# Performance work log

Hardware: AMD Instinct MI355X
Metric: run time of the kernel (lower is better)

## Reference

```python
import jax, jax.numpy as jnp
import numpy as np

TEMPERATURE = 1.0 / 0.07  # fixed (temperature_trainable=False)
B, D = 256, 65536


def setup_inputs() -> dict:
    key = jax.random.key(0)
    kA, kB = jax.random.split(key)
    feat_A = jax.random.normal(kA, (B, D), dtype=jnp.float32)
    feat_B = jax.random.normal(kB, (B, D), dtype=jnp.float32)
    # L2-normalize (standard for contrastive features; keeps exp(logits) finite)
    feat_A = feat_A / jnp.linalg.norm(feat_A, axis=-1, keepdims=True)
    feat_B = feat_B / jnp.linalg.norm(feat_B, axis=-1, keepdims=True)
    return {"feat_A": feat_A, "feat_B": feat_B}


def reference(feat_A, feat_B):
    # logits[i, j] = <A_i, B_j> * temperature   -- [B, B]
    logits = jnp.einsum("id,jd->ij", feat_A, feat_B) * TEMPERATURE
    pos_logits = jnp.diagonal(logits)  # [B]
    # margin=0.0, dcl=False, index=None -> neg_mask is all True, so
    # log(sum_j exp(logits)) is a full-row/col logsumexp (stable form of exp->sum->log)
    neg_A2B = jax.nn.logsumexp(logits, axis=1)  # A -> B classification
    neg_B2A = jax.nn.logsumexp(logits, axis=0)  # B -> A classification
    loss_A2B = jnp.mean(neg_A2B - pos_logits)
    loss_B2A = jnp.mean(neg_B2A - pos_logits)
    return (loss_A2B + loss_B2A) * 0.5
```

## Files before the change

### kernel.cpp

```cpp
#include <hip/hip_runtime.h>
#include <hip/hip_bf16.h>


#define D_DIM 65536
#define B_DIM 256
#define LDK 72

constexpr float TEMP = 1.0f / 0.07f;

typedef short short8 __attribute__((ext_vector_type(8)));
typedef float floatx4 __attribute__((ext_vector_type(4)));

__device__ inline unsigned short f2bf(float f) {
  unsigned u = __builtin_bit_cast(unsigned, f);
  unsigned rounding = 0x7fffu + ((u >> 16) & 1u);
  return (unsigned short)((u + rounding) >> 16);
}

__device__ inline void st_bf16x4(unsigned short* dst, float4 v) {
  uint2 u;
  u.x = (unsigned)f2bf(v.x) | ((unsigned)f2bf(v.y) << 16);
  u.y = (unsigned)f2bf(v.z) | ((unsigned)f2bf(v.w) << 16);
  *(uint2*)dst = u;
}

__global__ __launch_bounds__(256, 2) void gemm_splitk(
    const float* __restrict__ A, const float* __restrict__ Bm,
    float* __restrict__ partials, int Kc) {
  const int bid = blockIdx.x;
  const int mt = (bid & 1) * 128;
  const int nt = ((bid >> 1) & 1) * 128;
  const int chunk = bid >> 2;
  const size_t k0 = (size_t)chunk * (size_t)Kc;

  __shared__ unsigned short As[128][LDK];
  __shared__ unsigned short Bs[128][LDK];

  const int t = threadIdx.x;
  const int lane = t & 63;
  const int w = t >> 6;
  const int wm = (w & 1) * 64;
  const int wn = (w >> 1) * 64;

  const int lr = t >> 4;
  const int lc = (t & 15) * 4;

  const float* Abase = A + (size_t)(mt + lr) * D_DIM + k0 + lc;
  const float* Bbase = Bm + (size_t)(nt + lr) * D_DIM + k0 + lc;

  floatx4 acc[4][4];
#pragma unroll
  for (int mb = 0; mb < 4; ++mb)
#pragma unroll
    for (int nb = 0; nb < 4; ++nb) acc[mb][nb] = (floatx4)0.f;

  float4 ra[8], rb[8];
  const int nst = Kc >> 6;

#pragma unroll
  for (int p = 0; p < 8; ++p) {
    ra[p] = *(const float4*)(Abase + (size_t)p * 16 * D_DIM);
    rb[p] = *(const float4*)(Bbase + (size_t)p * 16 * D_DIM);
  }

  for (int s = 0; s < nst; ++s) {
#pragma unroll
    for (int p = 0; p < 8; ++p) {
      st_bf16x4(&As[lr + p * 16][lc], ra[p]);
      st_bf16x4(&Bs[lr + p * 16][lc], rb[p]);
    }
    __syncthreads();

    if (s + 1 < nst) {
      const float* Ap = Abase + (size_t)(s + 1) * 64;
      const float* Bp = Bbase + (size_t)(s + 1) * 64;
#pragma unroll
      for (int p = 0; p < 8; ++p) {
        ra[p] = *(const float4*)(Ap + (size_t)p * 16 * D_DIM);
        rb[p] = *(const float4*)(Bp + (size_t)p * 16 * D_DIM);
      }
    }

#pragma unroll
    for (int ks = 0; ks < 64; ks += 32) {
      short8 af[4], bf[4];
      const int ko = ks + (lane >> 4) * 8;
#pragma unroll
      for (int mb = 0; mb < 4; ++mb)
        af[mb] = *(const short8*)&As[wm + mb * 16 + (lane & 15)][ko];
#pragma unroll
      for (int nb = 0; nb < 4; ++nb)
        bf[nb] = *(const short8*)&Bs[wn + nb * 16 + (lane & 15)][ko];
#pragma unroll
      for (int mb = 0; mb < 4; ++mb)
#pragma unroll
        for (int nb = 0; nb < 4; ++nb)
          acc[mb][nb] = __builtin_amdgcn_mfma_f32_16x16x32_bf16(
              af[mb], bf[nb], acc[mb][nb], 0, 0, 0);
    }
    __syncthreads();
  }

  float* outp = partials + (size_t)chunk * (B_DIM * B_DIM);
#pragma unroll
  for (int mb = 0; mb < 4; ++mb) {
#pragma unroll
    for (int nb = 0; nb < 4; ++nb) {
      const int gi0 = mt + wm + mb * 16 + ((lane >> 4) * 4);
      const int gj = nt + wn + nb * 16 + (lane & 15);
#pragma unroll
      for (int r = 0; r < 4; ++r)
        outp[(size_t)(gi0 + r) * B_DIM + gj] = acc[mb][nb][r];
    }
  }
}

__global__ void reduce_rows(const float* __restrict__ partials,
                            float* __restrict__ logits,
                            float* __restrict__ out, int C) {
  const int i = blockIdx.x;
  const int j = threadIdx.x;
  const float* p = partials + (size_t)i * B_DIM + j;
  float s = 0.f;
#pragma unroll 4
  for (int c = 0; c < C; ++c) s += p[(size_t)c * (B_DIM * B_DIM)];
  const float lg = s * TEMP;
  logits[i * B_DIM + j] = lg;

  __shared__ float posv;
  if (j == i) posv = lg;

  float e = expf(lg);
#pragma unroll
  for (int off = 32; off > 0; off >>= 1) e += __shfl_down(e, off);
  __shared__ float wsum[4];
  if ((j & 63) == 0) wsum[j >> 6] = e;
  __syncthreads();
  if (j == 0) {
    const float tot = wsum[0] + wsum[1] + wsum[2] + wsum[3];
    atomicAdd(out, (logf(tot) - 2.f * posv) * (0.5f / 256.f));
  }
}

__global__ void reduce_cols(const float* __restrict__ logits,
                            float* __restrict__ out) {
  const int j = blockIdx.x;
  const int i = threadIdx.x;
  float e = expf(logits[(size_t)i * B_DIM + j]);
#pragma unroll
  for (int off = 32; off > 0; off >>= 1) e += __shfl_down(e, off);
  __shared__ float wsum[4];
  if ((i & 63) == 0) wsum[i >> 6] = e;
  __syncthreads();
  if (i == 0) {
    const float tot = wsum[0] + wsum[1] + wsum[2] + wsum[3];
    atomicAdd(out, logf(tot) * (0.5f / 256.f));
  }
}

extern "C" void kernel_launch(void* const* d_in, const int* in_sizes, int n_in,
                              void* d_out, int out_size, void* d_ws, size_t ws_size,
                              hipStream_t stream) {
  (void)in_sizes; (void)n_in; (void)out_size;
  const float* A = (const float*)d_in[0];
  const float* Bm = (const float*)d_in[1];
  float* out = (float*)d_out;

  const size_t per = (size_t)B_DIM * B_DIM * sizeof(float);
  int C = 128;
  while (C > 1 && (size_t)(C + 1) * per > ws_size) C >>= 1;
  const int Kc = D_DIM / C;

  float* logits = (float*)d_ws;
  float* partials = (float*)d_ws + (size_t)B_DIM * B_DIM;

  hipMemsetAsync(d_out, 0, sizeof(float), stream);
  gemm_splitk<<<4 * C, 256, 0, stream>>>(A, Bm, partials, Kc);
  reduce_rows<<<B_DIM, B_DIM, 0, stream>>>(partials, logits, out, C);
  reduce_cols<<<B_DIM, B_DIM, 0, stream>>>(logits, out);
}
```

Baseline: 174.3 us.

## Fuse split-K GEMM and logsumexp reductions into one cooperative kernel

Merges the split-K GEMM, the partial-sum reduction and the row/column logsumexp passes into a single cooperative kernel that uses grid-wide syncs between phases. The partial reduction is now spread across all threads in the grid rather than one block per row, and the work loop is persistent so the grid can be capped at the occupancy limit. The aim is to remove two kernel launches and their gaps. In exchange it adds grid sync overhead, and if occupancy caps the grid below 512 blocks, some blocks must process several GEMM tiles in turn.

```diff
diff --git a/kernel.cpp b/kernel.cpp
--- a/kernel.cpp
+++ b/kernel.cpp
@@ -1,5 +1,8 @@
 #include <hip/hip_runtime.h>
 #include <hip/hip_bf16.h>
+#include <hip/hip_cooperative_groups.h>
+
+namespace cg = cooperative_groups;
 
 
 #define D_DIM 65536
@@ -24,18 +27,12 @@
   *(uint2*)dst = u;
 }
 
-__global__ __launch_bounds__(256, 2) void gemm_splitk(
+__global__ __launch_bounds__(256, 2) void fused(
     const float* __restrict__ A, const float* __restrict__ Bm,
-    float* __restrict__ partials, int Kc) {
+    float* __restrict__ partials, float* __restrict__ logits,
+    float* __restrict__ out, int Kc, int C) {
   const int bid = blockIdx.x;
-  const int mt = (bid & 1) * 128;
-  const int nt = ((bid >> 1) & 1) * 128;
-  const int chunk = bid >> 2;
-  const size_t k0 = (size_t)chunk * (size_t)Kc;
-
-  __shared__ unsigned short As[128][LDK];
-  __shared__ unsigned short Bs[128][LDK];
-
+  const int nblocks = gridDim.x;
   const int t = threadIdx.x;
   const int lane = t & 63;
   const int w = t >> 6;
@@ -45,116 +42,127 @@
   const int lr = t >> 4;
   const int lc = (t & 15) * 4;
 
-  const float* Abase = A + (size_t)(mt + lr) * D_DIM + k0 + lc;
-  const float* Bbase = Bm + (size_t)(nt + lr) * D_DIM + k0 + lc;
-
-  floatx4 acc[4][4];
-#pragma unroll
-  for (int mb = 0; mb < 4; ++mb)
-#pragma unroll
-    for (int nb = 0; nb < 4; ++nb) acc[mb][nb] = (floatx4)0.f;
-
-  float4 ra[8], rb[8];
-  const int nst = Kc >> 6;
-
-#pragma unroll
-  for (int p = 0; p < 8; ++p) {
-    ra[p] = *(const float4*)(Abase + (size_t)p * 16 * D_DIM);
-    rb[p] = *(const float4*)(Bbase + (size_t)p * 16 * D_DIM);
-  }
-
-  for (int s = 0; s < nst; ++s) {
+  __shared__ unsigned short As[128][LDK];
+  __shared__ unsigned short Bs[128][LDK];
+
+  for (int wi = bid; wi < 4 * C; wi += nblocks) {
+    const int mt = (wi & 1) * 128;
+    const int nt = ((wi >> 1) & 1) * 128;
+    const int chunk = wi >> 2;
+    const size_t k0 = (size_t)chunk * (size_t)Kc;
+
+    const float* Abase = A + (size_t)(mt + lr) * D_DIM + k0 + lc;
+    const float* Bbase = Bm + (size_t)(nt + lr) * D_DIM + k0 + lc;
+
+    floatx4 acc[4][4];
+#pragma unroll
+    for (int mb = 0; mb < 4; ++mb)
+#pragma unroll
+      for (int nb = 0; nb < 4; ++nb) acc[mb][nb] = (floatx4)0.f;
+
+    float4 ra[8], rb[8];
+    const int nst = Kc >> 6;
+
 #pragma unroll
     for (int p = 0; p < 8; ++p) {
-      st_bf16x4(&As[lr + p * 16][lc], ra[p]);
-      st_bf16x4(&Bs[lr + p * 16][lc], rb[p]);
-    }
+      ra[p] = *(const float4*)(Abase + (size_t)p * 16 * D_DIM);
+      rb[p] = *(const float4*)(Bbase + (size_t)p * 16 * D_DIM);
+    }
+
+    for (int s = 0; s < nst; ++s) {
+#pragma unroll
+      for (int p = 0; p < 8; ++p) {
+        st_bf16x4(&As[lr + p * 16][lc], ra[p]);
+        st_bf16x4(&Bs[lr + p * 16][lc], rb[p]);
+      }
+      __syncthreads();
+
+      if (s + 1 < nst) {
+        const float* Ap = Abase + (size_t)(s + 1) * 64;
+        const float* Bp = Bbase + (size_t)(s + 1) * 64;
+#pragma unroll
+        for (int p = 0; p < 8; ++p) {
+          ra[p] = *(const float4*)(Ap + (size_t)p * 16 * D_DIM);
+          rb[p] = *(const float4*)(Bp + (size_t)p * 16 * D_DIM);
+        }
+      }
+
+#pragma unroll
+      for (int ks = 0; ks < 64; ks += 32) {
+        short8 af[4], bf[4];
+        const int ko = ks + (lane >> 4) * 8;
+#pragma unroll
+        for (int mb = 0; mb < 4; ++mb)
+          af[mb] = *(const short8*)&As[wm + mb * 16 + (lane & 15)][ko];
+#pragma unroll
+        for (int nb = 0; nb < 4; ++nb)
+          bf[nb] = *(const short8*)&Bs[wn + nb * 16 + (lane & 15)][ko];
+#pragma unroll
+        for (int mb = 0; mb < 4; ++mb)
+#pragma unroll
+          for (int nb = 0; nb < 4; ++nb)
+            acc[mb][nb] = __builtin_amdgcn_mfma_f32_16x16x32_bf16(
+                af[mb], bf[nb], acc[mb][nb], 0, 0, 0);
+      }
+      __syncthreads();
+    }
+
+    float* outp = partials + (size_t)chunk * (B_DIM * B_DIM);
+#pragma unroll
+    for (int mb = 0; mb < 4; ++mb) {
+#pragma unroll
+      for (int nb = 0; nb < 4; ++nb) {
+        const int gi0 = mt + wm + mb * 16 + ((lane >> 4) * 4);
+        const int gj = nt + wn + nb * 16 + (lane & 15);
+#pragma unroll
+        for (int r = 0; r < 4; ++r)
+          outp[(size_t)(gi0 + r) * B_DIM + gj] = acc[mb][nb][r];
+      }
+    }
+  }
+
+  __threadfence();
+  cg::this_grid().sync();
+
+  {
+    const int nthr = nblocks * 256;
+    for (int g = bid * 256 + t; g < B_DIM * B_DIM; g += nthr) {
+      const float* p = partials + g;
+      float s = 0.f;
+#pragma unroll 16
+      for (int c = 0; c < C; ++c) s += p[(size_t)c * (B_DIM * B_DIM)];
+      logits[g] = s * TEMP;
+    }
+  }
+
+  __threadfence();
+  cg::this_grid().sync();
+
+  __shared__ float wsum[4];
+  __shared__ float posv;
+  for (int task = bid; task < 2 * B_DIM; task += nblocks) {
     __syncthreads();
-
-    if (s + 1 < nst) {
-      const float* Ap = Abase + (size_t)(s + 1) * 64;
-      const float* Bp = Bbase + (size_t)(s + 1) * 64;
-#pragma unroll
-      for (int p = 0; p < 8; ++p) {
-        ra[p] = *(const float4*)(Ap + (size_t)p * 16 * D_DIM);
-        rb[p] = *(const float4*)(Bp + (size_t)p * 16 * D_DIM);
-      }
-    }
-
-#pragma unroll
-    for (int ks = 0; ks < 64; ks += 32) {
-      short8 af[4], bf[4];
-      const int ko = ks + (lane >> 4) * 8;
-#pragma unroll
-      for (int mb = 0; mb < 4; ++mb)
-        af[mb] = *(const short8*)&As[wm + mb * 16 + (lane & 15)][ko];
-#pragma unroll
-      for (int nb = 0; nb < 4; ++nb)
-        bf[nb] = *(const short8*)&Bs[wn + nb * 16 + (lane & 15)][ko];
-#pragma unroll
-      for (int mb = 0; mb < 4; ++mb)
-#pragma unroll
-        for (int nb = 0; nb < 4; ++nb)
-          acc[mb][nb] = __builtin_amdgcn_mfma_f32_16x16x32_bf16(
-              af[mb], bf[nb], acc[mb][nb], 0, 0, 0);
+    float lg;
+    if (task < B_DIM) {
+      const int i = task;
+      lg = logits[i * B_DIM + t];
+      if (t == i) posv = lg;
+    } else {
+      const int j = task - B_DIM;
+      lg = logits[t * B_DIM + j];
     }
     __syncthreads();
-  }
-
-  float* outp = partials + (size_t)chunk * (B_DIM * B_DIM);
-#pragma unroll
-  for (int mb = 0; mb < 4; ++mb) {
-#pragma unroll
-    for (int nb = 0; nb < 4; ++nb) {
-      const int gi0 = mt + wm + mb * 16 + ((lane >> 4) * 4);
-      const int gj = nt + wn + nb * 16 + (lane & 15);
-#pragma unroll
-      for (int r = 0; r < 4; ++r)
-        outp[(size_t)(gi0 + r) * B_DIM + gj] = acc[mb][nb][r];
-    }
-  }
-}
-
-__global__ void reduce_rows(const float* __restrict__ partials,
-                            float* __restrict__ logits,
-                            float* __restrict__ out, int C) {
-  const int i = blockIdx.x;
-  const int j = threadIdx.x;
-  const float* p = partials + (size_t)i * B_DIM + j;
-  float s = 0.f;
-#pragma unroll 4
-  for (int c = 0; c < C; ++c) s += p[(size_t)c * (B_DIM * B_DIM)];
-  const float lg = s * TEMP;
-  logits[i * B_DIM + j] = lg;
-
-  __shared__ float posv;
-  if (j == i) posv = lg;
-
-  float e = expf(lg);
-#pragma unroll
-  for (int off = 32; off > 0; off >>= 1) e += __shfl_down(e, off);
-  __shared__ float wsum[4];
-  if ((j & 63) == 0) wsum[j >> 6] = e;
-  __syncthreads();
-  if (j == 0) {
-    const float tot = wsum[0] + wsum[1] + wsum[2] + wsum[3];
-    atomicAdd(out, (logf(tot) - 2.f * posv) * (0.5f / 256.f));
-  }
-}
-
-__global__ void reduce_cols(const float* __restrict__ logits,
-                            float* __restrict__ out) {
-  const int j = blockIdx.x;
-  const int i = threadIdx.x;
-  float e = expf(logits[(size_t)i * B_DIM + j]);
-#pragma unroll
-  for (int off = 32; off > 0; off >>= 1) e += __shfl_down(e, off);
-  __shared__ float wsum[4];
-  if ((i & 63) == 0) wsum[i >> 6] = e;
-  __syncthreads();
-  if (i == 0) {
-    const float tot = wsum[0] + wsum[1] + wsum[2] + wsum[3];
-    atomicAdd(out, logf(tot) * (0.5f / 256.f));
+    float e = expf(lg);
+#pragma unroll
+    for (int off = 32; off > 0; off >>= 1) e += __shfl_down(e, off);
+    if ((t & 63) == 0) wsum[t >> 6] = e;
+    __syncthreads();
+    if (t == 0) {
+      const float tot = wsum[0] + wsum[1] + wsum[2] + wsum[3];
+      float v = logf(tot) * (0.5f / 256.f);
+      if (task < B_DIM) v -= posv * (2.f * 0.5f / 256.f);
+      atomicAdd(out, v);
+    }
   }
 }
 
@@ -169,13 +177,24 @@
   const size_t per = (size_t)B_DIM * B_DIM * sizeof(float);
   int C = 128;
   while (C > 1 && (size_t)(C + 1) * per > ws_size) C >>= 1;
-  const int Kc = D_DIM / C;
+  int Kc = D_DIM / C;
 
   float* logits = (float*)d_ws;
   float* partials = (float*)d_ws + (size_t)B_DIM * B_DIM;
 
+  static int maxgrid = 0;
+  if (maxgrid == 0) {
+    int dev = 0, nb = 0, ncu = 0;
+    hipGetDevice(&dev);
+    hipOccupancyMaxActiveBlocksPerMultiprocessor(&nb, fused, 256, 0);
+    hipDeviceGetAttribute(&ncu, hipDeviceAttributeMultiprocessorCount, dev);
+    maxgrid = (nb > 0 && ncu > 0) ? nb * ncu : 512;
+  }
+  int grid = 4 * C;
+  if (grid > maxgrid) grid = maxgrid;
+
   hipMemsetAsync(d_out, 0, sizeof(float), stream);
-  gemm_splitk<<<4 * C, 256, 0, stream>>>(A, Bm, partials, Kc);
-  reduce_rows<<<B_DIM, B_DIM, 0, stream>>>(partials, logits, out, C);
-  reduce_cols<<<B_DIM, B_DIM, 0, stream>>>(logits, out);
-}
+  void* args[] = {(void*)&A, (void*)&Bm, (void*)&partials, (void*)&logits,
+                  (void*)&out, (void*)&Kc, (void*)&C};
+  hipLaunchCooperativeKernel(fused, dim3(grid), dim3(256), args, 0, stream);
+}
```

After: 310.9 us. 1.78x slower.

## Fuse row and column logsumexp reductions into one last-block finalize kernel

Applied to the files above, without the earlier changes.

Replaces the separate row-reduction and column-reduction kernels, and the memset of the output, with a single finalize kernel. Each block sums the split-K partials for one row using float4 loads split four ways over the chunks, then writes a per-row term. A global atomic counter picks the last block to finish, and that block computes the column logsumexps and writes the final loss directly. This removes one kernel launch and one memset. In exchange, the column pass now runs serially in a single block. The counter also relies on workspace state modulo 256, since it is never reset.

```diff
diff --git a/kernel.cpp b/kernel.cpp
--- a/kernel.cpp
+++ b/kernel.cpp
@@ -115,47 +115,63 @@
   }
 }
 
-__global__ void reduce_rows(const float* __restrict__ partials,
-                            float* __restrict__ logits,
-                            float* __restrict__ out, int C) {
-  const int i = blockIdx.x;
-  const int j = threadIdx.x;
-  const float* p = partials + (size_t)i * B_DIM + j;
-  float s = 0.f;
-#pragma unroll 4
-  for (int c = 0; c < C; ++c) s += p[(size_t)c * (B_DIM * B_DIM)];
-  const float lg = s * TEMP;
-  logits[i * B_DIM + j] = lg;
-
+__global__ __launch_bounds__(256) void finalize(
+    const float* __restrict__ partials, float* __restrict__ logits,
+    float* __restrict__ rowout, unsigned int* __restrict__ counter,
+    float* __restrict__ out, int C) {
+  const int b = blockIdx.x;
+  const int t = threadIdx.x;
+  const int q = t >> 6;
+  const int l = t & 63;
+
+  __shared__ float sums[4][B_DIM];
+  __shared__ float wsum[4];
   __shared__ float posv;
-  if (j == i) posv = lg;
+  __shared__ int lastflag;
+
+  float4 s4 = make_float4(0.f, 0.f, 0.f, 0.f);
+  const float* pb = partials + (size_t)b * B_DIM + 4 * l;
+#pragma unroll 8
+  for (int c = q; c < C; c += 4) {
+    const float4 v = *(const float4*)(pb + (size_t)c * (B_DIM * B_DIM));
+    s4.x += v.x;
+    s4.y += v.y;
+    s4.z += v.z;
+    s4.w += v.w;
+  }
+  *(float4*)&sums[q][4 * l] = s4;
+  __syncthreads();
+
+  const float lg = (sums[0][t] + sums[1][t] + sums[2][t] + sums[3][t]) * TEMP;
+  logits[b * B_DIM + t] = lg;
+  if (t == b) posv = lg;
 
   float e = expf(lg);
 #pragma unroll
   for (int off = 32; off > 0; off >>= 1) e += __shfl_down(e, off);
-  __shared__ float wsum[4];
-  if ((j & 63) == 0) wsum[j >> 6] = e;
-  __syncthreads();
-  if (j == 0) {
+  if (l == 0) wsum[q] = e;
+  __syncthreads();
+  if (t == 0) {
     const float tot = wsum[0] + wsum[1] + wsum[2] + wsum[3];
-    atomicAdd(out, (logf(tot) - 2.f * posv) * (0.5f / 256.f));
-  }
-}
-
-__global__ void reduce_cols(const float* __restrict__ logits,
-                            float* __restrict__ out) {
-  const int j = blockIdx.x;
-  const int i = threadIdx.x;
-  float e = expf(logits[(size_t)i * B_DIM + j]);
-#pragma unroll
-  for (int off = 32; off > 0; off >>= 1) e += __shfl_down(e, off);
-  __shared__ float wsum[4];
-  if ((i & 63) == 0) wsum[i >> 6] = e;
-  __syncthreads();
-  if (i == 0) {
-    const float tot = wsum[0] + wsum[1] + wsum[2] + wsum[3];
-    atomicAdd(out, logf(tot) * (0.5f / 256.f));
-  }
+    rowout[b] = logf(tot) - 2.f * posv;
+    __threadfence();
+    const unsigned old = atomicAdd(counter, 1u);
+    lastflag = (((old + 1u) & 255u) == 0u);
+    __threadfence();
+  }
+  __syncthreads();
+  if (!lastflag) return;
+
+  float csum = 0.f;
+#pragma unroll 8
+  for (int i = 0; i < B_DIM; ++i) csum += expf(logits[i * B_DIM + t]);
+  float v = rowout[t] + logf(csum);
+#pragma unroll
+  for (int off = 32; off > 0; off >>= 1) v += __shfl_down(v, off);
+  if (l == 0) wsum[q] = v;
+  __syncthreads();
+  if (t == 0)
+    out[0] = (wsum[0] + wsum[1] + wsum[2] + wsum[3]) * (0.5f / 256.f);
 }
 
 extern "C" void kernel_launch(void* const* d_in, const int* in_sizes, int n_in,
@@ -168,14 +184,17 @@
 
   const size_t per = (size_t)B_DIM * B_DIM * sizeof(float);
   int C = 128;
-  while (C > 1 && (size_t)(C + 1) * per > ws_size) C >>= 1;
+  while (C > 1 &&
+         (size_t)(C + 1) * per + (B_DIM + 16) * sizeof(float) > ws_size)
+    C >>= 1;
   const int Kc = D_DIM / C;
 
   float* logits = (float*)d_ws;
   float* partials = (float*)d_ws + (size_t)B_DIM * B_DIM;
-
-  hipMemsetAsync(d_out, 0, sizeof(float), stream);
+  float* rowout = partials + (size_t)C * B_DIM * B_DIM;
+  unsigned int* counter = (unsigned int*)(rowout + B_DIM);
+
   gemm_splitk<<<4 * C, 256, 0, stream>>>(A, Bm, partials, Kc);
-  reduce_rows<<<B_DIM, B_DIM, 0, stream>>>(partials, logits, out, C);
-  reduce_cols<<<B_DIM, B_DIM, 0, stream>>>(logits, out);
-}
+  finalize<<<B_DIM, B_DIM, 0, stream>>>(partials, logits, rowout, counter, out,
+                                        C);
+}
```

Result: slower. 180.1 us (+3.4%).
